# Optimization experiments

Measured on AMD Instinct MI355X. Metric: run time of the kernel, lower is better.

## Reference

```python
import jax, jax.numpy as jnp
import numpy as np

LAMBDA = 0.7
K = 3
HIDDEN = 8
IN_F = 512
OUT_F = 256
N = 4096


def _gat_layer(x, adj, W, a):
    # h = fc(x); e[i,j] = attn([h_i ; h_j]) = h_i @ a[:F] + h_j @ a[F:]
    # (same math as the N*N repeat/cat/linear, without materializing [N*N, 2F])
    h = x @ W                      # [N, F]
    F_ = h.shape[1]
    src = h @ a[:F_]               # [N, 1]
    dst = h @ a[F_:]               # [N, 1]
    e = src + dst.T                # [N, N]
    att = jax.nn.softmax(e, axis=1) * adj
    return jax.nn.elu(att @ h)     # [N, F]


def setup_inputs() -> dict:
    key = jax.random.key(0)
    ks = jax.random.split(key, 8)
    x = jax.random.normal(ks[0], (N, IN_F), dtype=jnp.float32)
    # binarized sparse-ish adjacency stored densely (avg degree ~41)
    adj = (jax.random.uniform(ks[1], (N, N)) < 0.01).astype(jnp.float32)
    W1 = jax.random.normal(ks[2], (IN_F, HIDDEN), dtype=jnp.float32) * (1.0 / np.sqrt(IN_F))
    a1 = jax.random.normal(ks[3], (2 * HIDDEN, 1), dtype=jnp.float32) * (1.0 / np.sqrt(2 * HIDDEN))
    W2 = jax.random.normal(ks[4], (HIDDEN, 1), dtype=jnp.float32) * (1.0 / np.sqrt(HIDDEN))
    a2 = jax.random.normal(ks[5], (2, 1), dtype=jnp.float32)
    W_sgc = jax.random.normal(ks[6], (IN_F * K, OUT_F), dtype=jnp.float32) * (1.0 / np.sqrt(IN_F * K))
    b_sgc = jnp.zeros((OUT_F,), dtype=jnp.float32)
    return {"x": x, "adj": adj, "W1": W1, "a1": a1, "W2": W2, "a2": a2,
            "W_sgc": W_sgc, "b_sgc": b_sgc}


def reference(x, adj, W1, a1, W2, a2, W_sgc, b_sgc):
    # GAT scoring head (dropout p=0.6 is identity at inference)
    h1 = _gat_layer(x, adj, W1, a1)
    node_scores = _gat_layer(h1, adj, W2, a2)        # [N, 1]

    # K-hop adjacency powers
    adj_list = [adj]
    for _ in range(1, K):
        adj_list.append(adj_list[-1] @ adj)

    # dynamic per-row masking (row-broadcast of node_scores > lambda)
    change_mask = (node_scores > LAMBDA).astype(adj.dtype)  # [N, 1] broadcasts over cols
    for k in range(K - 1):
        adj_list[k] = adj_list[k] * change_mask
        adj_list[k + 1] = adj_list[k + 1] * (1.0 - change_mask)

    # SGC: concat K hop-aggregated features, then linear
    agg = jnp.concatenate([A @ x for A in adj_list], axis=1)  # [N, K*IN_F]
    return agg @ W_sgc + b_sgc
```

## Files before the change

### kernel.cpp

```cpp
#include <hip/hip_runtime.h>
#include <hip/hip_bf16.h>
#include <cstddef>

#define NNODE 4096
#define INF   512
#define OUTF  256
#define HID   8
#define CAP   128

typedef __attribute__((ext_vector_type(8))) short short8;
typedef __attribute__((ext_vector_type(4))) float f32x4;

__device__ __forceinline__ unsigned short f2bf(float f){
  unsigned int u = __float_as_uint(f);
  u += 0x7fffu + ((u >> 16) & 1u);
  return (unsigned short)(u >> 16);
}
__device__ __forceinline__ float bf2f(unsigned short s){
  return __uint_as_float((unsigned int)s << 16);
}

#define HOP_LOAD(buf, b) { int _o = (b) * 16 + half;                          \
  _Pragma("unroll") for (int t = 0; t < 8; t++){                              \
    int _j = cl[_o + 2 * t];                                                  \
    buf[t] = *(const short8*)(src + (size_t)_j * instride); } }
#define HOP_CONS(buf) { _Pragma("unroll") for (int t = 0; t < 8; t++)         \
  _Pragma("unroll") for (int e = 0; e < 8; e++)                               \
    acc[e] += bf2f((unsigned short)buf[t][e]); }
#define HOP_PIPE() {                                                          \
  if (nb > 0){                                                                \
    HOP_LOAD(pA, 0);                                                          \
    int i = 1;                                                                \
    for (; i + 1 < nb; i += 2){                                               \
      HOP_LOAD(pB, i);                                                        \
      HOP_CONS(pA);                                                           \
      HOP_LOAD(pA, i + 1);                                                    \
      HOP_CONS(pB);                                                           \
    }                                                                         \
    if (i < nb){ HOP_LOAD(pB, i); HOP_CONS(pA); HOP_CONS(pB); }               \
    else { HOP_CONS(pA); }                                                    \
  } }

__global__ __launch_bounds__(256) void front(const float* __restrict__ adj,
                                             int* __restrict__ deg,
                                             int* __restrict__ cols,
                                             const float* __restrict__ x,
                                             const float* __restrict__ W1,
                                             const float* __restrict__ a1,
                                             float* __restrict__ h,
                                             float* __restrict__ dstv,
                                             unsigned short* __restrict__ xb,
                                             const float* __restrict__ Wsgc,
                                             unsigned short* __restrict__ wbT,
                                             unsigned short* __restrict__ Gb,
                                             unsigned short* __restrict__ T1,
                                             unsigned short* __restrict__ T2){
  __shared__ int cnt;
  int bid = blockIdx.x, tid = threadIdx.x;
  int lane = tid & 63;

  if (bid < NNODE){
    int row = bid;
    if (tid == 0) cnt = 0;
    __syncthreads();
    const float4* arow = (const float4*)(adj + (size_t)row * NNODE);
    int* crow = cols + (size_t)row * CAP;
    #pragma unroll
    for (int k = 0; k < 4; k++){
      int idx = k * 256 + tid;
      float4 v = arow[idx];
      int n0 = (v.x != 0.f), n1 = (v.y != 0.f), n2 = (v.z != 0.f), n3 = (v.w != 0.f);
      int m = n0 + n1 + n2 + n3;
      int pre = m;
      #pragma unroll
      for (int o = 1; o < 64; o <<= 1){
        int t = __shfl_up(pre, o, 64);
        if (lane >= o) pre += t;
      }
      int wtot = __shfl(pre, 63, 64);
      int base = 0;
      if (lane == 63 && wtot) base = atomicAdd(&cnt, wtot);
      base = __shfl(base, 63, 64);
      int o = base + pre - m;
      int c = idx * 4;
      if (n0){ if (o < CAP) crow[o] = c;     o++; }
      if (n1){ if (o < CAP) crow[o] = c + 1; o++; }
      if (n2){ if (o < CAP) crow[o] = c + 2; o++; }
      if (n3){ if (o < CAP) crow[o] = c + 3; }
    }
    __syncthreads();
    int c = cnt > CAP ? CAP : cnt;
    int c16 = (c + 15) & ~15;
    if (c16 == 0) c16 = 16;
    if (c16 > CAP) c16 = CAP;
    if (tid < c16 - c) crow[c + tid] = NNODE;
    if (tid == 0) deg[row] = c16;

  } else if (bid < NNODE + 1024){
    int b2 = bid - NNODE;
    if (b2 == 0 && tid < HID) h[(size_t)NNODE * HID + tid] = 0.f;
    int wave = tid >> 6;
    int row = b2 * 4 + wave;
    const float* xr8 = x + (size_t)row * INF + lane * 8;
    float4 v0 = ((const float4*)xr8)[0];
    float4 v1 = ((const float4*)xr8)[1];
    float xv[8] = {v0.x, v0.y, v0.z, v0.w, v1.x, v1.y, v1.z, v1.w};
    union { short8 v; unsigned short u[8]; } pk;
    #pragma unroll
    for (int u = 0; u < 8; u++) pk.u[u] = f2bf(xv[u]);
    *(short8*)(xb + (size_t)row * INF + lane * 8) = pk.v;
    float acc[HID];
    #pragma unroll
    for (int f = 0; f < HID; f++) acc[f] = 0.f;
    #pragma unroll
    for (int u = 0; u < 8; u++){
      const float* wp = W1 + (size_t)(lane * 8 + u) * HID;
      #pragma unroll
      for (int f = 0; f < HID; f++) acc[f] += xv[u] * wp[f];
    }
    #pragma unroll
    for (int f = 0; f < HID; f++)
      for (int o = 32; o >= 1; o >>= 1) acc[f] += __shfl_xor(acc[f], o, 64);
    if (lane == 0){
      float d = 0.f;
      #pragma unroll
      for (int f = 0; f < HID; f++){ h[(size_t)row*HID + f] = acc[f]; d += acc[f] * a1[HID + f]; }
      dstv[row] = d;
    }

  } else {
    int idx = (bid - NNODE - 1024) * 256 + tid;
    if (idx < 512) Gb[(size_t)NNODE * 512 + idx] = 0;
    if (idx < 256){ T1[(size_t)NNODE * 256 + idx] = 0; T2[(size_t)NNODE * 256 + idx] = 0; }
    int c = idx >> 9, k = idx & 511;
    float val = (c < 256) ? Wsgc[(size_t)k * OUTF + c]
                          : Wsgc[(size_t)(1024 + k) * OUTF + (c - 256)];
    wbT[idx] = f2bf(val);
  }
}

__global__ __launch_bounds__(256) void mid(const unsigned short* __restrict__ XB,
                                           const unsigned short* __restrict__ BT,
                                           unsigned short* __restrict__ Gb,
                                           const float* __restrict__ h,
                                           const float* __restrict__ dstv,
                                           const int* __restrict__ deg,
                                           const int* __restrict__ cols,
                                           const float* __restrict__ W2,
                                           float* __restrict__ h2){
  __shared__ union {
    struct { unsigned short As[128][72]; unsigned short Bs[128][72]; } g;
    struct { float p[NNODE + 1]; float red[4]; } a;
  } sm;
  int bid = blockIdx.x, tid = threadIdx.x;
  int wave = tid >> 6, lane = tid & 63;

  if (bid < 128){
    int bx = bid & 31, by = bid >> 5;
    int row0 = bx * 128, col0 = by * 128;
    int wr = wave >> 1, wc = wave & 1;
    f32x4 acc[4][4];
    #pragma unroll
    for (int i = 0; i < 4; i++)
      #pragma unroll
      for (int j = 0; j < 4; j++)
        #pragma unroll
        for (int e = 0; e < 4; e++) acc[i][j][e] = 0.f;
    int mrow = lane & 15;
    int kq = (lane >> 4) * 8;
    for (int k0 = 0; k0 < 512; k0 += 64){
      #pragma unroll
      for (int ps = 0; ps < 4; ps++){
        int idx = ps * 256 + tid;
        int r = idx >> 3;
        int ko = (idx & 7) * 8;
        *(int4*)(&sm.g.As[r][ko]) = *(const int4*)(XB + ((size_t)(row0 + r) * 512 + k0 + ko));
        *(int4*)(&sm.g.Bs[r][ko]) = *(const int4*)(BT + ((size_t)(col0 + r) * 512 + k0 + ko));
      }
      __syncthreads();
      #pragma unroll
      for (int kk = 0; kk < 2; kk++){
        short8 a[4], b[4];
        #pragma unroll
        for (int i = 0; i < 4; i++)
          a[i] = *(const short8*)(&sm.g.As[wr * 64 + i * 16 + mrow][kk * 32 + kq]);
        #pragma unroll
        for (int j = 0; j < 4; j++)
          b[j] = *(const short8*)(&sm.g.Bs[wc * 64 + j * 16 + mrow][kk * 32 + kq]);
        #pragma unroll
        for (int i = 0; i < 4; i++)
          #pragma unroll
          for (int j = 0; j < 4; j++)
            acc[i][j] = __builtin_amdgcn_mfma_f32_16x16x32_bf16(a[i], b[j], acc[i][j], 0, 0, 0);
      }
      __syncthreads();
    }
    int crow = (lane >> 4) * 4;
    int ccol = lane & 15;
    #pragma unroll
    for (int i = 0; i < 4; i++)
      #pragma unroll
      for (int j = 0; j < 4; j++)
        #pragma unroll
        for (int e = 0; e < 4; e++){
          int r = row0 + wr * 64 + i * 16 + crow + e;
          int c = col0 + wc * 64 + j * 16 + ccol;
          Gb[(size_t)r * 512 + c] = f2bf(acc[i][j][e]);
        }

  } else {
    if (tid == 0) sm.a.p[NNODE] = 0.f;
    float mx = -INFINITY;
    for (int i = tid; i < NNODE; i += 256) mx = fmaxf(mx, dstv[i]);
    #pragma unroll
    for (int o = 32; o >= 1; o >>= 1) mx = fmaxf(mx, __shfl_xor(mx, o, 64));
    if (lane == 0) sm.a.red[wave] = mx;
    __syncthreads();
    mx = fmaxf(fmaxf(sm.a.red[0], sm.a.red[1]), fmaxf(sm.a.red[2], sm.a.red[3]));
    __syncthreads();
    float sum = 0.f;
    for (int i = tid; i < NNODE; i += 256){ float e = expf(dstv[i] - mx); sm.a.p[i] = e; sum += e; }
    #pragma unroll
    for (int o = 32; o >= 1; o >>= 1) sum += __shfl_xor(sum, o, 64);
    if (lane == 0) sm.a.red[wave] = sum;
    __syncthreads();
    float inv = 1.0f / (sm.a.red[0] + sm.a.red[1] + sm.a.red[2] + sm.a.red[3]);
    for (int i = tid; i < NNODE; i += 256) sm.a.p[i] *= inv;
    __syncthreads();

    int row = (bid - 128) * 4 + wave;
    const int* cl = cols + (size_t)row * CAP;
    int d = deg[row];
    int ng = lane >> 3;
    int f  = lane & 7;
    float acc = 0.f;
    for (int n = ng; n < d; n += 8){
      int j = cl[n];
      acc += sm.a.p[j] * h[(size_t)j * HID + f];
    }
    acc += __shfl_xor(acc, 8, 64);
    acc += __shfl_xor(acc, 16, 64);
    acc += __shfl_xor(acc, 32, 64);
    float e = acc > 0.f ? acc : expm1f(acc);
    float t = e * W2[f];
    t += __shfl_xor(t, 1, 64);
    t += __shfl_xor(t, 2, 64);
    t += __shfl_xor(t, 4, 64);
    if (lane == 0) h2[row] = t;
  }
}

__global__ __launch_bounds__(256, 4) void sc_hop1(const unsigned short* __restrict__ Gb,
                                                  unsigned short* __restrict__ T1,
                                                  const float* __restrict__ h2,
                                                  const float* __restrict__ a2,
                                                  const int* __restrict__ deg,
                                                  const int* __restrict__ cols,
                                                  float* __restrict__ maskf){
  __shared__ float q[NNODE + 1];
  __shared__ float red[4];
  int bid = blockIdx.x, tid = threadIdx.x;
  int wave = tid >> 6, lane = tid & 63;

  if (bid < 1024){
    int row = bid * 4 + wave;
    const int* cl = cols + (size_t)row * CAP;
    int nb = deg[row] >> 4;
    int half = lane >> 5, cid = lane & 31;
    const int instride = 512;
    const unsigned short* src = Gb + 256 + cid * 8;
    float acc[8];
    #pragma unroll
    for (int e = 0; e < 8; e++) acc[e] = 0.f;
    short8 pA[8], pB[8];
    HOP_PIPE();
    #pragma unroll
    for (int e = 0; e < 8; e++) acc[e] += __shfl_xor(acc[e], 32, 64);
    if (half == 0){
      union { short8 v; unsigned short u[8]; } pk;
      #pragma unroll
      for (int e = 0; e < 8; e++) pk.u[e] = f2bf(acc[e]);
      *(short8*)(T1 + (size_t)row * OUTF + cid * 8) = pk.v;
    }

  } else {
    float s2 = a2[1];
    if (tid == 0) q[NNODE] = 0.f;
    float mx = -INFINITY;
    for (int i = tid; i < NNODE; i += 256) mx = fmaxf(mx, s2 * h2[i]);
    #pragma unroll
    for (int o = 32; o >= 1; o >>= 1) mx = fmaxf(mx, __shfl_xor(mx, o, 64));
    if (lane == 0) red[wave] = mx;
    __syncthreads();
    mx = fmaxf(fmaxf(red[0], red[1]), fmaxf(red[2], red[3]));
    __syncthreads();
    float sum = 0.f;
    for (int i = tid; i < NNODE; i += 256){ float e = expf(s2 * h2[i] - mx); q[i] = e; sum += e; }
    #pragma unroll
    for (int o = 32; o >= 1; o >>= 1) sum += __shfl_xor(sum, o, 64);
    if (lane == 0) red[wave] = sum;
    __syncthreads();
    float inv = 1.0f / (red[0] + red[1] + red[2] + red[3]);
    for (int i = tid; i < NNODE; i += 256) q[i] = q[i] * inv * h2[i];
    __syncthreads();

    int row = (bid - 1024) * 4 + wave;
    const int* cl = cols + (size_t)row * CAP;
    int d = deg[row];
    float s = 0.f;
    for (int n = lane; n < d; n += 64) s += q[cl[n]];
    #pragma unroll
    for (int o = 32; o >= 1; o >>= 1) s += __shfl_xor(s, o, 64);
    if (lane == 0){
      float e = s > 0.f ? s : expm1f(s);
      maskf[row] = (e > 0.7f) ? 1.0f : 0.0f;
    }
  }
}

__global__ __launch_bounds__(256, 4) void hop_bf(const unsigned short* __restrict__ in,
                                                 int instride, int colbase,
                                                 unsigned short* __restrict__ out,
                                                 const int* __restrict__ deg,
                                                 const int* __restrict__ cols){
  int wave = threadIdx.x >> 6, lane = threadIdx.x & 63;
  int row = blockIdx.x * 4 + wave;
  const int* cl = cols + (size_t)row * CAP;
  int nb = deg[row] >> 4;
  int half = lane >> 5, cid = lane & 31;
  const unsigned short* src = in + colbase + cid * 8;
  float acc[8];
  #pragma unroll
  for (int e = 0; e < 8; e++) acc[e] = 0.f;
  short8 pA[8], pB[8];
  HOP_PIPE();
  #pragma unroll
  for (int e = 0; e < 8; e++) acc[e] += __shfl_xor(acc[e], 32, 64);
  if (half == 0){
    union { short8 v; unsigned short u[8]; } pk;
    #pragma unroll
    for (int e = 0; e < 8; e++) pk.u[e] = f2bf(acc[e]);
    *(short8*)(out + (size_t)row * OUTF + cid * 8) = pk.v;
  }
}

__global__ __launch_bounds__(256, 4) void hop_final_bf(const unsigned short* __restrict__ Gb,
                                                       const unsigned short* __restrict__ T2,
                                                       const float* __restrict__ maskf,
                                                       const float* __restrict__ b,
                                                       float* __restrict__ out,
                                                       const int* __restrict__ deg,
                                                       const int* __restrict__ cols){
  int wave = threadIdx.x >> 6, lane = threadIdx.x & 63;
  int row = blockIdx.x * 4 + wave;
  const int* cl = cols + (size_t)row * CAP;
  int nb = deg[row] >> 4;
  bool m = maskf[row] != 0.0f;
  const unsigned short* base = m ? Gb : T2;
  int instride = m ? 512 : 256;
  int half = lane >> 5, cid = lane & 31;
  const unsigned short* src = base + cid * 8;
  float acc[8];
  #pragma unroll
  for (int e = 0; e < 8; e++) acc[e] = 0.f;
  short8 pA[8], pB[8];
  HOP_PIPE();
  #pragma unroll
  for (int e = 0; e < 8; e++) acc[e] += __shfl_xor(acc[e], 32, 64);
  if (half == 0){
    f32x4 b0 = ((const f32x4*)(b + cid * 8))[0];
    f32x4 b1 = ((const f32x4*)(b + cid * 8 + 4))[0];
    f32x4 o0, o1;
    #pragma unroll
    for (int e = 0; e < 4; e++){ o0[e] = acc[e] + b0[e]; o1[e] = acc[4 + e] + b1[e]; }
    float* orow = out + (size_t)row * OUTF + cid * 8;
    ((f32x4*)orow)[0] = o0;
    ((f32x4*)(orow + 4))[0] = o1;
  }
}

extern "C" void kernel_launch(void* const* d_in, const int* in_sizes, int n_in,
                              void* d_out, int out_size, void* d_ws, size_t ws_size,
                              hipStream_t stream) {
  const float* x    = (const float*)d_in[0];
  const float* adj  = (const float*)d_in[1];
  const float* W1   = (const float*)d_in[2];
  const float* a1   = (const float*)d_in[3];
  const float* W2   = (const float*)d_in[4];
  const float* a2   = (const float*)d_in[5];
  const float* Wsgc = (const float*)d_in[6];
  const float* bsgc = (const float*)d_in[7];
  float* out = (float*)d_out;

  char* w = (char*)d_ws;
  size_t off = 0;
  auto carve = [&](size_t bytes) -> char* {
    char* p = w + off;
    off += (bytes + 255) & ~(size_t)255;
    return p;
  };
  int*   deg   = (int*)carve((size_t)NNODE * 4);
  int*   cols  = (int*)carve((size_t)NNODE * CAP * 4);
  float* h     = (float*)carve((size_t)(NNODE + 1) * HID * 4);
  float* dstv  = (float*)carve((size_t)NNODE * 4);
  float* h2    = (float*)carve((size_t)NNODE * 4);
  float* maskf = (float*)carve((size_t)NNODE * 4);
  unsigned short* wbT = (unsigned short*)carve((size_t)512 * 512 * 2);
  unsigned short* xb  = (unsigned short*)carve((size_t)NNODE * INF * 2);
  unsigned short* Gb  = (unsigned short*)carve((size_t)(NNODE + 1) * 512 * 2);
  unsigned short* T1  = (unsigned short*)carve((size_t)(NNODE + 1) * OUTF * 2);
  unsigned short* T2  = (unsigned short*)carve((size_t)(NNODE + 1) * OUTF * 2);

  front<<<NNODE + 1024 + 1024, 256, 0, stream>>>(adj, deg, cols,
                                                 x, W1, a1, h, dstv, xb,
                                                 Wsgc, wbT, Gb, T1, T2);
  mid<<<128 + 1024, 256, 0, stream>>>(xb, wbT, Gb, h, dstv, deg, cols, W2, h2);
  sc_hop1<<<2048, 256, 0, stream>>>(Gb, T1, h2, a2, deg, cols, maskf);
  hop_bf<<<NNODE / 4, 256, 0, stream>>>(T1, 256, 0, T2, deg, cols);
  hop_final_bf<<<NNODE / 4, 256, 0, stream>>>(Gb, T2, maskf, bsgc, out, deg, cols);
}
```

Baseline: 174.2 us.

## Merge five kernels into one cooperative persistent kernel with grid syncs

```diff
diff --git a/kernel.cpp b/kernel.cpp
--- a/kernel.cpp
+++ b/kernel.cpp
@@ -1,12 +1,15 @@
 #include <hip/hip_runtime.h>
-#include <hip/hip_bf16.h>
+#include <hip/hip_cooperative_groups.h>
 #include <cstddef>
+
+namespace cg = cooperative_groups;
 
 #define NNODE 4096
 #define INF   512
 #define OUTF  256
 #define HID   8
 #define CAP   128
+#define GRID  512
 
 typedef __attribute__((ext_vector_type(8))) short short8;
 typedef __attribute__((ext_vector_type(4))) float f32x4;
@@ -20,177 +23,165 @@
   return __uint_as_float((unsigned int)s << 16);
 }
 
-#define HOP_LOAD(buf, b) { int _o = (b) * 16 + half;                          \
-  _Pragma("unroll") for (int t = 0; t < 8; t++){                              \
-    int _j = cl[_o + 2 * t];                                                  \
-    buf[t] = *(const short8*)(src + (size_t)_j * instride); } }
-#define HOP_CONS(buf) { _Pragma("unroll") for (int t = 0; t < 8; t++)         \
-  _Pragma("unroll") for (int e = 0; e < 8; e++)                               \
-    acc[e] += bf2f((unsigned short)buf[t][e]); }
-#define HOP_PIPE() {                                                          \
-  if (nb > 0){                                                                \
-    HOP_LOAD(pA, 0);                                                          \
-    int i = 1;                                                                \
-    for (; i + 1 < nb; i += 2){                                               \
-      HOP_LOAD(pB, i);                                                        \
-      HOP_CONS(pA);                                                           \
-      HOP_LOAD(pA, i + 1);                                                    \
-      HOP_CONS(pB);                                                           \
-    }                                                                         \
-    if (i < nb){ HOP_LOAD(pB, i); HOP_CONS(pA); HOP_CONS(pB); }               \
-    else { HOP_CONS(pA); }                                                    \
-  } }
-
-__global__ __launch_bounds__(256) void front(const float* __restrict__ adj,
-                                             int* __restrict__ deg,
-                                             int* __restrict__ cols,
-                                             const float* __restrict__ x,
-                                             const float* __restrict__ W1,
-                                             const float* __restrict__ a1,
-                                             float* __restrict__ h,
-                                             float* __restrict__ dstv,
-                                             unsigned short* __restrict__ xb,
-                                             const float* __restrict__ Wsgc,
-                                             unsigned short* __restrict__ wbT,
-                                             unsigned short* __restrict__ Gb,
-                                             unsigned short* __restrict__ T1,
-                                             unsigned short* __restrict__ T2){
-  __shared__ int cnt;
-  int bid = blockIdx.x, tid = threadIdx.x;
-  int lane = tid & 63;
-
-  if (bid < NNODE){
-    int row = bid;
-    if (tid == 0) cnt = 0;
-    __syncthreads();
-    const float4* arow = (const float4*)(adj + (size_t)row * NNODE);
-    int* crow = cols + (size_t)row * CAP;
-    #pragma unroll
-    for (int k = 0; k < 4; k++){
-      int idx = k * 256 + tid;
-      float4 v = arow[idx];
-      int n0 = (v.x != 0.f), n1 = (v.y != 0.f), n2 = (v.z != 0.f), n3 = (v.w != 0.f);
-      int m = n0 + n1 + n2 + n3;
-      int pre = m;
-      #pragma unroll
-      for (int o = 1; o < 64; o <<= 1){
-        int t = __shfl_up(pre, o, 64);
-        if (lane >= o) pre += t;
-      }
-      int wtot = __shfl(pre, 63, 64);
-      int base = 0;
-      if (lane == 63 && wtot) base = atomicAdd(&cnt, wtot);
-      base = __shfl(base, 63, 64);
-      int o = base + pre - m;
-      int c = idx * 4;
-      if (n0){ if (o < CAP) crow[o] = c;     o++; }
-      if (n1){ if (o < CAP) crow[o] = c + 1; o++; }
-      if (n2){ if (o < CAP) crow[o] = c + 2; o++; }
-      if (n3){ if (o < CAP) crow[o] = c + 3; }
-    }
-    __syncthreads();
-    int c = cnt > CAP ? CAP : cnt;
-    int c16 = (c + 15) & ~15;
-    if (c16 == 0) c16 = 16;
-    if (c16 > CAP) c16 = CAP;
-    if (tid < c16 - c) crow[c + tid] = NNODE;
-    if (tid == 0) deg[row] = c16;
-
-  } else if (bid < NNODE + 1024){
-    int b2 = bid - NNODE;
-    if (b2 == 0 && tid < HID) h[(size_t)NNODE * HID + tid] = 0.f;
-    int wave = tid >> 6;
-    int row = b2 * 4 + wave;
-    const float* xr8 = x + (size_t)row * INF + lane * 8;
-    float4 v0 = ((const float4*)xr8)[0];
-    float4 v1 = ((const float4*)xr8)[1];
-    float xv[8] = {v0.x, v0.y, v0.z, v0.w, v1.x, v1.y, v1.z, v1.w};
-    union { short8 v; unsigned short u[8]; } pk;
-    #pragma unroll
-    for (int u = 0; u < 8; u++) pk.u[u] = f2bf(xv[u]);
-    *(short8*)(xb + (size_t)row * INF + lane * 8) = pk.v;
-    float acc[HID];
-    #pragma unroll
-    for (int f = 0; f < HID; f++) acc[f] = 0.f;
-    #pragma unroll
-    for (int u = 0; u < 8; u++){
-      const float* wp = W1 + (size_t)(lane * 8 + u) * HID;
-      #pragma unroll
-      for (int f = 0; f < HID; f++) acc[f] += xv[u] * wp[f];
-    }
-    #pragma unroll
-    for (int f = 0; f < HID; f++)
-      for (int o = 32; o >= 1; o >>= 1) acc[f] += __shfl_xor(acc[f], o, 64);
-    if (lane == 0){
-      float d = 0.f;
-      #pragma unroll
-      for (int f = 0; f < HID; f++){ h[(size_t)row*HID + f] = acc[f]; d += acc[f] * a1[HID + f]; }
-      dstv[row] = d;
-    }
-
-  } else {
-    int idx = (bid - NNODE - 1024) * 256 + tid;
-    if (idx < 512) Gb[(size_t)NNODE * 512 + idx] = 0;
-    if (idx < 256){ T1[(size_t)NNODE * 256 + idx] = 0; T2[(size_t)NNODE * 256 + idx] = 0; }
-    int c = idx >> 9, k = idx & 511;
-    float val = (c < 256) ? Wsgc[(size_t)k * OUTF + c]
-                          : Wsgc[(size_t)(1024 + k) * OUTF + (c - 256)];
-    wbT[idx] = f2bf(val);
-  }
-}
-
-__global__ __launch_bounds__(256) void mid(const unsigned short* __restrict__ XB,
-                                           const unsigned short* __restrict__ BT,
-                                           unsigned short* __restrict__ Gb,
-                                           const float* __restrict__ h,
-                                           const float* __restrict__ dstv,
-                                           const int* __restrict__ deg,
-                                           const int* __restrict__ cols,
-                                           const float* __restrict__ W2,
-                                           float* __restrict__ h2){
+__device__ __forceinline__ void hop_accum(const unsigned short* __restrict__ src,
+                                          int instride, const int* __restrict__ cl,
+                                          int nb, int half, float* acc){
+  for (int i = 0; i < nb; i++){
+    short8 v[8];
+    #pragma unroll
+    for (int t = 0; t < 8; t++){
+      int j = cl[i * 16 + half + 2 * t];
+      v[t] = *(const short8*)(src + (size_t)j * instride);
+    }
+    #pragma unroll
+    for (int t = 0; t < 8; t++)
+      #pragma unroll
+      for (int e = 0; e < 8; e++)
+        acc[e] += bf2f((unsigned short)v[t][e]);
+  }
+}
+
+__global__ __launch_bounds__(256, 2) void coop(
+    const float* __restrict__ adj,
+    int* __restrict__ deg, int* __restrict__ cols,
+    const float* __restrict__ x, const float* __restrict__ W1,
+    const float* __restrict__ a1, float* __restrict__ h,
+    float* __restrict__ dstv, unsigned short* __restrict__ xb,
+    const float* __restrict__ Wsgc, unsigned short* __restrict__ wbT,
+    unsigned short* __restrict__ Gb, unsigned short* __restrict__ T1,
+    unsigned short* __restrict__ T2, const float* __restrict__ W2,
+    float* __restrict__ h2, const float* __restrict__ a2,
+    float* __restrict__ maskf, const float* __restrict__ bsgc,
+    float* __restrict__ out)
+{
   __shared__ union {
-    struct { unsigned short As[128][72]; unsigned short Bs[128][72]; } g;
-    struct { float p[NNODE + 1]; float red[4]; } a;
+    int cnt;
+    struct { unsigned short As[128][72]; unsigned short Bs[64][72]; } g;
+    struct { float v[NNODE + 1]; float red[4]; } sx;
   } sm;
-  int bid = blockIdx.x, tid = threadIdx.x;
-  int wave = tid >> 6, lane = tid & 63;
-
-  if (bid < 128){
+  cg::grid_group gg = cg::this_grid();
+  const int bid = blockIdx.x, tid = threadIdx.x;
+  const int wave = tid >> 6, lane = tid & 63;
+
+  for (int t = bid; t < NNODE + 1024 + 1024; t += GRID){
+    if (t < NNODE){
+      int row = t;
+      if (tid == 0) sm.cnt = 0;
+      __syncthreads();
+      const float4* arow = (const float4*)(adj + (size_t)row * NNODE);
+      int* crow = cols + (size_t)row * CAP;
+      #pragma unroll
+      for (int k = 0; k < 4; k++){
+        int idx = k * 256 + tid;
+        float4 v = arow[idx];
+        int n0 = (v.x != 0.f), n1 = (v.y != 0.f), n2 = (v.z != 0.f), n3 = (v.w != 0.f);
+        int m = n0 + n1 + n2 + n3;
+        int pre = m;
+        #pragma unroll
+        for (int o = 1; o < 64; o <<= 1){
+          int tt = __shfl_up(pre, o, 64);
+          if (lane >= o) pre += tt;
+        }
+        int wtot = __shfl(pre, 63, 64);
+        int base = 0;
+        if (lane == 63 && wtot) base = atomicAdd(&sm.cnt, wtot);
+        base = __shfl(base, 63, 64);
+        int o2 = base + pre - m;
+        int c = idx * 4;
+        if (n0){ if (o2 < CAP) crow[o2] = c;     o2++; }
+        if (n1){ if (o2 < CAP) crow[o2] = c + 1; o2++; }
+        if (n2){ if (o2 < CAP) crow[o2] = c + 2; o2++; }
+        if (n3){ if (o2 < CAP) crow[o2] = c + 3; }
+      }
+      __syncthreads();
+      int c = sm.cnt > CAP ? CAP : sm.cnt;
+      int c16 = (c + 15) & ~15;
+      if (c16 == 0) c16 = 16;
+      if (c16 > CAP) c16 = CAP;
+      if (tid < c16 - c) crow[c + tid] = NNODE;
+      if (tid == 0) deg[row] = c16;
+      __syncthreads();
+    } else if (t < NNODE + 1024){
+      int gt = t - NNODE;
+      if (gt == 0 && tid < HID) h[(size_t)NNODE * HID + tid] = 0.f;
+      int row = gt * 4 + wave;
+      const float* xr8 = x + (size_t)row * INF + lane * 8;
+      float4 v0 = ((const float4*)xr8)[0];
+      float4 v1 = ((const float4*)xr8)[1];
+      float xv[8] = {v0.x, v0.y, v0.z, v0.w, v1.x, v1.y, v1.z, v1.w};
+      union { short8 v; unsigned short u[8]; } pk;
+      #pragma unroll
+      for (int u = 0; u < 8; u++) pk.u[u] = f2bf(xv[u]);
+      *(short8*)(xb + (size_t)row * INF + lane * 8) = pk.v;
+      float acc[HID];
+      #pragma unroll
+      for (int f = 0; f < HID; f++) acc[f] = 0.f;
+      #pragma unroll
+      for (int u = 0; u < 8; u++){
+        const float* wp = W1 + (size_t)(lane * 8 + u) * HID;
+        #pragma unroll
+        for (int f = 0; f < HID; f++) acc[f] += xv[u] * wp[f];
+      }
+      #pragma unroll
+      for (int f = 0; f < HID; f++)
+        for (int o = 32; o >= 1; o >>= 1) acc[f] += __shfl_xor(acc[f], o, 64);
+      if (lane == 0){
+        float d = 0.f;
+        #pragma unroll
+        for (int f = 0; f < HID; f++){ h[(size_t)row*HID + f] = acc[f]; d += acc[f] * a1[HID + f]; }
+        dstv[row] = d;
+      }
+    } else {
+      int idx = (t - NNODE - 1024) * 256 + tid;
+      if (idx < 512) Gb[(size_t)NNODE * 512 + idx] = 0;
+      if (idx < 256){ T1[(size_t)NNODE * 256 + idx] = 0; T2[(size_t)NNODE * 256 + idx] = 0; }
+      int c = idx >> 9, k = idx & 511;
+      float val = (c < 256) ? Wsgc[(size_t)k * OUTF + c]
+                            : Wsgc[(size_t)(1024 + k) * OUTF + (c - 256)];
+      wbT[idx] = f2bf(val);
+    }
+  }
+  __threadfence(); gg.sync();
+
+  if (bid < 256){
     int bx = bid & 31, by = bid >> 5;
-    int row0 = bx * 128, col0 = by * 128;
+    int row0 = bx * 128, col0 = by * 64;
     int wr = wave >> 1, wc = wave & 1;
-    f32x4 acc[4][4];
+    f32x4 acc[4][2];
     #pragma unroll
     for (int i = 0; i < 4; i++)
       #pragma unroll
-      for (int j = 0; j < 4; j++)
+      for (int j = 0; j < 2; j++)
         #pragma unroll
         for (int e = 0; e < 4; e++) acc[i][j][e] = 0.f;
-    int mrow = lane & 15;
-    int kq = (lane >> 4) * 8;
+    int mrow = lane & 15, kq = (lane >> 4) * 8;
     for (int k0 = 0; k0 < 512; k0 += 64){
       #pragma unroll
       for (int ps = 0; ps < 4; ps++){
         int idx = ps * 256 + tid;
-        int r = idx >> 3;
-        int ko = (idx & 7) * 8;
-        *(int4*)(&sm.g.As[r][ko]) = *(const int4*)(XB + ((size_t)(row0 + r) * 512 + k0 + ko));
-        *(int4*)(&sm.g.Bs[r][ko]) = *(const int4*)(BT + ((size_t)(col0 + r) * 512 + k0 + ko));
+        int r = idx >> 3, ko = (idx & 7) * 8;
+        *(int4*)(&sm.g.As[r][ko]) = *(const int4*)(xb + ((size_t)(row0 + r) * 512 + k0 + ko));
+      }
+      #pragma unroll
+      for (int ps = 0; ps < 2; ps++){
+        int idx = ps * 256 + tid;
+        int c = idx >> 3, ko = (idx & 7) * 8;
+        *(int4*)(&sm.g.Bs[c][ko]) = *(const int4*)(wbT + ((size_t)(col0 + c) * 512 + k0 + ko));
       }
       __syncthreads();
       #pragma unroll
       for (int kk = 0; kk < 2; kk++){
-        short8 a[4], b[4];
+        short8 a[4], b[2];
         #pragma unroll
         for (int i = 0; i < 4; i++)
           a[i] = *(const short8*)(&sm.g.As[wr * 64 + i * 16 + mrow][kk * 32 + kq]);
         #pragma unroll
-        for (int j = 0; j < 4; j++)
-          b[j] = *(const short8*)(&sm.g.Bs[wc * 64 + j * 16 + mrow][kk * 32 + kq]);
+        for (int j = 0; j < 2; j++)
+          b[j] = *(const short8*)(&sm.g.Bs[wc * 32 + j * 16 + mrow][kk * 32 + kq]);
         #pragma unroll
         for (int i = 0; i < 4; i++)
           #pragma unroll
-          for (int j = 0; j < 4; j++)
+          for (int j = 0; j < 2; j++)
             acc[i][j] = __builtin_amdgcn_mfma_f32_16x16x32_bf16(a[i], b[j], acc[i][j], 0, 0, 0);
       }
       __syncthreads();
@@ -200,80 +191,68 @@
     #pragma unroll
     for (int i = 0; i < 4; i++)
       #pragma unroll
-      for (int j = 0; j < 4; j++)
+      for (int j = 0; j < 2; j++)
         #pragma unroll
         for (int e = 0; e < 4; e++){
           int r = row0 + wr * 64 + i * 16 + crow + e;
-          int c = col0 + wc * 64 + j * 16 + ccol;
+          int c = col0 + wc * 32 + j * 16 + ccol;
           Gb[(size_t)r * 512 + c] = f2bf(acc[i][j][e]);
         }
-
-  } else {
-    if (tid == 0) sm.a.p[NNODE] = 0.f;
+  }
+  __syncthreads();
+  {
+    if (tid == 0) sm.sx.v[NNODE] = 0.f;
     float mx = -INFINITY;
     for (int i = tid; i < NNODE; i += 256) mx = fmaxf(mx, dstv[i]);
     #pragma unroll
     for (int o = 32; o >= 1; o >>= 1) mx = fmaxf(mx, __shfl_xor(mx, o, 64));
-    if (lane == 0) sm.a.red[wave] = mx;
-    __syncthreads();
-    mx = fmaxf(fmaxf(sm.a.red[0], sm.a.red[1]), fmaxf(sm.a.red[2], sm.a.red[3]));
+    if (lane == 0) sm.sx.red[wave] = mx;
+    __syncthreads();
+    mx = fmaxf(fmaxf(sm.sx.red[0], sm.sx.red[1]), fmaxf(sm.sx.red[2], sm.sx.red[3]));
     __syncthreads();
     float sum = 0.f;
-    for (int i = tid; i < NNODE; i += 256){ float e = expf(dstv[i] - mx); sm.a.p[i] = e; sum += e; }
+    for (int i = tid; i < NNODE; i += 256){ float e = expf(dstv[i] - mx); sm.sx.v[i] = e; sum += e; }
     #pragma unroll
     for (int o = 32; o >= 1; o >>= 1) sum += __shfl_xor(sum, o, 64);
-    if (lane == 0) sm.a.red[wave] = sum;
-    __syncthreads();
-    float inv = 1.0f / (sm.a.red[0] + sm.a.red[1] + sm.a.red[2] + sm.a.red[3]);
-    for (int i = tid; i < NNODE; i += 256) sm.a.p[i] *= inv;
-    __syncthreads();
-
-    int row = (bid - 128) * 4 + wave;
-    const int* cl = cols + (size_t)row * CAP;
-    int d = deg[row];
-    int ng = lane >> 3;
-    int f  = lane & 7;
-    float acc = 0.f;
-    for (int n = ng; n < d; n += 8){
-      int j = cl[n];
-      acc += sm.a.p[j] * h[(size_t)j * HID + f];
-    }
-    acc += __shfl_xor(acc, 8, 64);
-    acc += __shfl_xor(acc, 16, 64);
-    acc += __shfl_xor(acc, 32, 64);
-    float e = acc > 0.f ? acc : expm1f(acc);
-    float t = e * W2[f];
-    t += __shfl_xor(t, 1, 64);
-    t += __shfl_xor(t, 2, 64);
-    t += __shfl_xor(t, 4, 64);
-    if (lane == 0) h2[row] = t;
-  }
-}
-
-__global__ __launch_bounds__(256, 4) void sc_hop1(const unsigned short* __restrict__ Gb,
-                                                  unsigned short* __restrict__ T1,
-                                                  const float* __restrict__ h2,
-                                                  const float* __restrict__ a2,
-                                                  const int* __restrict__ deg,
-                                                  const int* __restrict__ cols,
-                                                  float* __restrict__ maskf){
-  __shared__ float q[NNODE + 1];
-  __shared__ float red[4];
-  int bid = blockIdx.x, tid = threadIdx.x;
-  int wave = tid >> 6, lane = tid & 63;
-
-  if (bid < 1024){
-    int row = bid * 4 + wave;
+    if (lane == 0) sm.sx.red[wave] = sum;
+    __syncthreads();
+    float inv = 1.0f / (sm.sx.red[0] + sm.sx.red[1] + sm.sx.red[2] + sm.sx.red[3]);
+    for (int i = tid; i < NNODE; i += 256) sm.sx.v[i] *= inv;
+    __syncthreads();
+    for (int t = bid; t < 1280; t += GRID){
+      if (t < 256) continue;
+      int row = (t - 256) * 4 + wave;
+      const int* cl = cols + (size_t)row * CAP;
+      int d = deg[row];
+      int ng = lane >> 3, f = lane & 7;
+      float acc = 0.f;
+      for (int n = ng; n < d; n += 8){
+        int j = cl[n];
+        acc += sm.sx.v[j] * h[(size_t)j * HID + f];
+      }
+      acc += __shfl_xor(acc, 8, 64);
+      acc += __shfl_xor(acc, 16, 64);
+      acc += __shfl_xor(acc, 32, 64);
+      float e = acc > 0.f ? acc : expm1f(acc);
+      float tt = e * W2[f];
+      tt += __shfl_xor(tt, 1, 64);
+      tt += __shfl_xor(tt, 2, 64);
+      tt += __shfl_xor(tt, 4, 64);
+      if (lane == 0) h2[row] = tt;
+    }
+  }
+  __threadfence(); gg.sync();
+
+  for (int t = bid; t < 1024; t += GRID){
+    int row = t * 4 + wave;
     const int* cl = cols + (size_t)row * CAP;
     int nb = deg[row] >> 4;
     int half = lane >> 5, cid = lane & 31;
-    const int instride = 512;
     const unsigned short* src = Gb + 256 + cid * 8;
     float acc[8];
     #pragma unroll
     for (int e = 0; e < 8; e++) acc[e] = 0.f;
-    short8 pA[8], pB[8];
-    HOP_PIPE();
+    hop_accum(src, 512, cl, nb, half, acc);
     #pragma unroll
     for (int e = 0; e < 8; e++) acc[e] += __shfl_xor(acc[e], 32, 64);
     if (half == 0){
@@ -282,100 +261,90 @@
       for (int e = 0; e < 8; e++) pk.u[e] = f2bf(acc[e]);
       *(short8*)(T1 + (size_t)row * OUTF + cid * 8) = pk.v;
     }
-
-  } else {
+  }
+  __syncthreads();
+  {
     float s2 = a2[1];
-    if (tid == 0) q[NNODE] = 0.f;
+    if (tid == 0) sm.sx.v[NNODE] = 0.f;
     float mx = -INFINITY;
     for (int i = tid; i < NNODE; i += 256) mx = fmaxf(mx, s2 * h2[i]);
     #pragma unroll
     for (int o = 32; o >= 1; o >>= 1) mx = fmaxf(mx, __shfl_xor(mx, o, 64));
-    if (lane == 0) red[wave] = mx;
-    __syncthreads();
-    mx = fmaxf(fmaxf(red[0], red[1]), fmaxf(red[2], red[3]));
+    if (lane == 0) sm.sx.red[wave] = mx;
+    __syncthreads();
+    mx = fmaxf(fmaxf(sm.sx.red[0], sm.sx.red[1]), fmaxf(sm.sx.red[2], sm.sx.red[3]));
     __syncthreads();
     float sum = 0.f;
-    for (int i = tid; i < NNODE; i += 256){ float e = expf(s2 * h2[i] - mx); q[i] = e; sum += e; }
+    for (int i = tid; i < NNODE; i += 256){ float e = expf(s2 * h2[i] - mx); sm.sx.v[i] = e; sum += e; }
     #pragma unroll
     for (int o = 32; o >= 1; o >>= 1) sum += __shfl_xor(sum, o, 64);
-    if (lane == 0) red[wave] = sum;
-    __syncthreads();
-    float inv = 1.0f / (red[0] + red[1] + red[2] + red[3]);
-    for (int i = tid; i < NNODE; i += 256) q[i] = q[i] * inv * h2[i];
-    __syncthreads();
-
-    int row = (bid - 1024) * 4 + wave;
+    if (lane == 0) sm.sx.red[wave] = sum;
+    __syncthreads();
+    float inv = 1.0f / (sm.sx.red[0] + sm.sx.red[1] + sm.sx.red[2] + sm.sx.red[3]);
+    for (int i = tid; i < NNODE; i += 256) sm.sx.v[i] = sm.sx.v[i] * inv * h2[i];
+    __syncthreads();
+    for (int t = bid; t < 1024; t += GRID){
+      int row = t * 4 + wave;
+      const int* cl = cols + (size_t)row * CAP;
+      int d = deg[row];
+      float s = 0.f;
+      for (int n = lane; n < d; n += 64) s += sm.sx.v[cl[n]];
+      #pragma unroll
+      for (int o = 32; o >= 1; o >>= 1) s += __shfl_xor(s, o, 64);
+      if (lane == 0){
+        float e = s > 0.f ? s : expm1f(s);
+        maskf[row] = (e > 0.7f) ? 1.0f : 0.0f;
+      }
+    }
+  }
+  __threadfence(); gg.sync();
+
+  for (int t = bid; t < 1024; t += GRID){
+    int row = t * 4 + wave;
     const int* cl = cols + (size_t)row * CAP;
-    int d = deg[row];
-    float s = 0.f;
-    for (int n = lane; n < d; n += 64) s += q[cl[n]];
-    #pragma unroll
-    for (int o = 32; o >= 1; o >>= 1) s += __shfl_xor(s, o, 64);
-    if (lane == 0){
-      float e = s > 0.f ? s : expm1f(s);
-      maskf[row] = (e > 0.7f) ? 1.0f : 0.0f;
-    }
-  }
-}
-
-__global__ __launch_bounds__(256, 4) void hop_bf(const unsigned short* __restrict__ in,
-                                                 int instride, int colbase,
-                                                 unsigned short* __restrict__ out,
-                                                 const int* __restrict__ deg,
-                                                 const int* __restrict__ cols){
-  int wave = threadIdx.x >> 6, lane = threadIdx.x & 63;
-  int row = blockIdx.x * 4 + wave;
-  const int* cl = cols + (size_t)row * CAP;
-  int nb = deg[row] >> 4;
-  int half = lane >> 5, cid = lane & 31;
-  const unsigned short* src = in + colbase + cid * 8;
-  float acc[8];
-  #pragma unroll
-  for (int e = 0; e < 8; e++) acc[e] = 0.f;
-  short8 pA[8], pB[8];
-  HOP_PIPE();
-  #pragma unroll
-  for (int e = 0; e < 8; e++) acc[e] += __shfl_xor(acc[e], 32, 64);
-  if (half == 0){
-    union { short8 v; unsigned short u[8]; } pk;
-    #pragma unroll
-    for (int e = 0; e < 8; e++) pk.u[e] = f2bf(acc[e]);
-    *(short8*)(out + (size_t)row * OUTF + cid * 8) = pk.v;
-  }
-}
-
-__global__ __launch_bounds__(256, 4) void hop_final_bf(const unsigned short* __restrict__ Gb,
-                                                       const unsigned short* __restrict__ T2,
-                                                       const float* __restrict__ maskf,
-                                                       const float* __restrict__ b,
-                                                       float* __restrict__ out,
-                                                       const int* __restrict__ deg,
-                                                       const int* __restrict__ cols){
-  int wave = threadIdx.x >> 6, lane = threadIdx.x & 63;
-  int row = blockIdx.x * 4 + wave;
-  const int* cl = cols + (size_t)row * CAP;
-  int nb = deg[row] >> 4;
-  bool m = maskf[row] != 0.0f;
-  const unsigned short* base = m ? Gb : T2;
-  int instride = m ? 512 : 256;
-  int half = lane >> 5, cid = lane & 31;
-  const unsigned short* src = base + cid * 8;
-  float acc[8];
-  #pragma unroll
-  for (int e = 0; e < 8; e++) acc[e] = 0.f;
-  short8 pA[8], pB[8];
-  HOP_PIPE();
-  #pragma unroll
-  for (int e = 0; e < 8; e++) acc[e] += __shfl_xor(acc[e], 32, 64);
-  if (half == 0){
-    f32x4 b0 = ((const f32x4*)(b + cid * 8))[0];
-    f32x4 b1 = ((const f32x4*)(b + cid * 8 + 4))[0];
-    f32x4 o0, o1;
-    #pragma unroll
-    for (int e = 0; e < 4; e++){ o0[e] = acc[e] + b0[e]; o1[e] = acc[4 + e] + b1[e]; }
-    float* orow = out + (size_t)row * OUTF + cid * 8;
-    ((f32x4*)orow)[0] = o0;
-    ((f32x4*)(orow + 4))[0] = o1;
+    int nb = deg[row] >> 4;
+    int half = lane >> 5, cid = lane & 31;
+    const unsigned short* src = T1 + cid * 8;
+    float acc[8];
+    #pragma unroll
+    for (int e = 0; e < 8; e++) acc[e] = 0.f;
+    hop_accum(src, 256, cl, nb, half, acc);
+    #pragma unroll
+    for (int e = 0; e < 8; e++) acc[e] += __shfl_xor(acc[e], 32, 64);
+    if (half == 0){
+      union { short8 v; unsigned short u[8]; } pk;
+      #pragma unroll
+      for (int e = 0; e < 8; e++) pk.u[e] = f2bf(acc[e]);
+      *(short8*)(T2 + (size_t)row * OUTF + cid * 8) = pk.v;
+    }
+  }
+  __threadfence(); gg.sync();
+
+  for (int t = bid; t < 1024; t += GRID){
+    int row = t * 4 + wave;
+    const int* cl = cols + (size_t)row * CAP;
+    int nb = deg[row] >> 4;
+    bool m = maskf[row] != 0.0f;
+    const unsigned short* base = m ? Gb : T2;
+    int instride = m ? 512 : 256;
+    int half = lane >> 5, cid = lane & 31;
+    const unsigned short* src = base + cid * 8;
+    float acc[8];
+    #pragma unroll
+    for (int e = 0; e < 8; e++) acc[e] = 0.f;
+    hop_accum(src, instride, cl, nb, half, acc);
+    #pragma unroll
+    for (int e = 0; e < 8; e++) acc[e] += __shfl_xor(acc[e], 32, 64);
+    if (half == 0){
+      f32x4 b0 = ((const f32x4*)(bsgc + cid * 8))[0];
+      f32x4 b1 = ((const f32x4*)(bsgc + cid * 8 + 4))[0];
+      f32x4 o0, o1;
+      #pragma unroll
+      for (int e = 0; e < 4; e++){ o0[e] = acc[e] + b0[e]; o1[e] = acc[4 + e] + b1[e]; }
+      float* orow = out + (size_t)row * OUTF + cid * 8;
+      ((f32x4*)orow)[0] = o0;
+      ((f32x4*)(orow + 4))[0] = o1;
+    }
   }
 }
 
@@ -411,11 +380,10 @@
   unsigned short* T1  = (unsigned short*)carve((size_t)(NNODE + 1) * OUTF * 2);
   unsigned short* T2  = (unsigned short*)carve((size_t)(NNODE + 1) * OUTF * 2);
 
-  front<<<NNODE + 1024 + 1024, 256, 0, stream>>>(adj, deg, cols,
-                                                 x, W1, a1, h, dstv, xb,
-                                                 Wsgc, wbT, Gb, T1, T2);
-  mid<<<128 + 1024, 256, 0, stream>>>(xb, wbT, Gb, h, dstv, deg, cols, W2, h2);
-  sc_hop1<<<2048, 256, 0, stream>>>(Gb, T1, h2, a2, deg, cols, maskf);
-  hop_bf<<<NNODE / 4, 256, 0, stream>>>(T1, 256, 0, T2, deg, cols);
-  hop_final_bf<<<NNODE / 4, 256, 0, stream>>>(Gb, T2, maskf, bsgc, out, deg, cols);
-}
+  void* args[] = {
+    (void*)&adj, (void*)&deg, (void*)&cols, (void*)&x, (void*)&W1, (void*)&a1,
+    (void*)&h, (void*)&dstv, (void*)&xb, (void*)&Wsgc, (void*)&wbT,
+    (void*)&Gb, (void*)&T1, (void*)&T2, (void*)&W2, (void*)&h2,
+    (void*)&a2, (void*)&maskf, (void*)&bsgc, (void*)&out };
+  hipLaunchCooperativeKernel((const void*)coop, dim3(GRID), dim3(256), args, 0, stream);
+}
```

After: 620.9 us. +256.3%, slower.
